# Optimization experiments

Measured on AMD Instinct MI355X. Metric: run time of the kernel, lower is better.

Reference implementation:

```python
import jax, jax.numpy as jnp
import numpy as np

SIGMA = 1e-2        # softness of the silhouette edge test, in NDC units (~1 pixel)
VIEW_ANGLE_DEG = 30.0  # NMR default perspective viewing angle
DIST_THRESHOLD = 6.0
EPS = 1e-7


def _normalize(v):
    return v / jnp.maximum(jnp.linalg.norm(v), 1e-8)


def setup_inputs() -> dict:
    key = jax.random.key(0)
    k1, k2, k3 = jax.random.split(key, 3)
    V, F, H, W = 1024, 2048, 192, 192
    vertices = 2.0 * jax.random.normal(k1, (1, V, 3), dtype=jnp.float32)
    faces = jax.random.randint(k2, (1, F, 3), 0, V, dtype=jnp.int32)
    image_ref = (jax.random.uniform(k3, (H, W), dtype=jnp.float32) > 0.5).astype(jnp.float32)
    camera_position = jnp.array([6.0, 10.0, -14.0], dtype=jnp.float32)
    return {"vertices": vertices, "faces": faces, "image_ref": image_ref,
            "camera_position": camera_position}


def _render_silhouette(vertices, faces, camera_position, H, W):
    dt = vertices.dtype
    # ---- look_at camera transform (NMR convention: at=origin, up=+y) ----
    eye = camera_position
    z_axis = _normalize(-eye)                      # toward the origin
    x_axis = _normalize(jnp.cross(jnp.array([0., 1., 0.], dt), z_axis))
    y_axis = jnp.cross(z_axis, x_axis)
    R = jnp.stack([x_axis, y_axis, z_axis])        # [3,3], rows = camera axes
    v_cam = (vertices[0] - eye) @ R.T              # [V,3]
    # ---- perspective projection to NDC ----
    ratio = jnp.tan(jnp.deg2rad(jnp.asarray(VIEW_ANGLE_DEG, dt)))
    z = jnp.maximum(v_cam[:, 2], 1e-5)
    xy = v_cam[:, :2] / (z[:, None] * ratio)       # [V,2] in [-1,1]
    # ---- gather per-face screen-space vertices ----
    fv = xy[faces[0]]                              # [F,3,2]  irregular gather
    edges = fv[:, [1, 2, 0], :] - fv               # [F,3,2]  edge vectors
    # edge-function constant: cross(edge, p - v) = ex*py - ey*px + (ey*vx - ex*vy)
    c = edges[..., 1] * fv[..., 0] - edges[..., 0] * fv[..., 1]          # [F,3]
    elen = jnp.maximum(jnp.linalg.norm(edges, axis=-1), 1e-8)            # [F,3]
    # orientation sign from signed twice-area so either winding counts as inside
    e01, e02 = fv[:, 1] - fv[:, 0], fv[:, 2] - fv[:, 0]
    area2 = e01[:, 0] * e02[:, 1] - e01[:, 1] * e02[:, 0]                # [F]
    sgn = jnp.where(area2 >= 0, 1.0, -1.0).astype(dt)                    # [F]
    # ---- pixel grid (NDC centers) ----
    xs = (jnp.arange(W, dtype=dt) + 0.5) / W * 2.0 - 1.0
    ys = 1.0 - (jnp.arange(H, dtype=dt) + 0.5) / H * 2.0
    px = xs[None, :]                               # broadcast to [H,W]
    py = ys[:, None]
    # ---- soft inside test: product of per-edge sigmoids of signed distance ----
    inside = jnp.ones((faces.shape[1], H, W), dt)
    for i in range(3):  # fixed small structural loop over triangle edges
        d = (edges[:, i, 0, None, None] * py
             - edges[:, i, 1, None, None] * px
             + c[:, i, None, None])                # [F,H,W]
        d = d * (sgn / elen[:, i])[:, None, None]  # normalized signed distance
        inside = inside * jax.nn.sigmoid(d / SIGMA)
    # silhouette = 1 - prod_f (1 - inside_f), accumulated in log space
    log_miss = jnp.sum(jnp.log(1.0 - inside + EPS), axis=0)  # [H,W]
    return 1.0 - jnp.exp(log_miss)


def reference(vertices, faces, image_ref, camera_position):
    H, W = image_ref.shape
    image = _render_silhouette(vertices, faces, camera_position, H, W)   # [H,W]
    distance = jnp.linalg.norm(camera_position)
    distance_penalty = jax.nn.relu(DIST_THRESHOLD - distance)
    loss = jnp.sum((image_ref - image) ** 2) * (1.0 + distance_penalty)
    return loss
```

## Files before the change

### kernel.cpp

```cpp
#include <hip/hip_runtime.h>

#define HH 192
#define WW 192
#define VV 1024
#define FF 2048
#define NPIX (HH*WW)
#define SIG 0.01f
#define EPSF 1e-7f
#define LOG2E 1.4426950408889634f
#define BAND_T 15.0f
#define C_OUT 1.4426943e-7f
#define C_IN  (-23.2534966642f)
#define NTILE 576


__global__ void __launch_bounds__(256)
prep_kernel(const float* __restrict__ verts, const int* __restrict__ faces,
            const float* __restrict__ cam, float* __restrict__ coeffs,
            float* __restrict__ logmiss, float* __restrict__ factor_out,
            float* __restrict__ out) {
    const int b = blockIdx.x, tid = threadIdx.x;
    if (b < NPIX / 256) {
        logmiss[b * 256 + tid] = 0.0f;
        return;
    }
    __shared__ float sx[VV], sy[VV];
    const float cx = cam[0], cy = cam[1], cz = cam[2];
    const float nrm = sqrtf(cx*cx + cy*cy + cz*cz);
    const float inv = 1.0f / fmaxf(nrm, 1e-8f);
    const float zx = -cx*inv, zy = -cy*inv, zz = -cz*inv;
    float xx = zz, xz = -zx;
    const float invx = 1.0f / fmaxf(sqrtf(xx*xx + xz*xz), 1e-8f);
    xx *= invx; xz *= invx;
    const float yx = zy*xz;
    const float yy = zz*xx - zx*xz;
    const float yz = -zy*xx;
    const float ratio = 0.57735026918962576f;

    for (int i = tid; i < VV; i += 256) {
        const float vx = verts[3*i+0] - cx;
        const float vy = verts[3*i+1] - cy;
        const float vz = verts[3*i+2] - cz;
        const float pcx = xx*vx + xz*vz;
        const float pcy = yx*vx + yy*vy + yz*vz;
        float pcz = zx*vx + zy*vy + zz*vz;
        pcz = fmaxf(pcz, 1e-5f);
        const float iz = 1.0f / (pcz * ratio);
        sx[i] = pcx * iz;
        sy[i] = pcy * iz;
    }
    __syncthreads();

    const int f = (b - 144) * 256 + tid;
    const int i0 = faces[3*f+0], i1 = faces[3*f+1], i2 = faces[3*f+2];
    const float p0x = sx[i0], p0y = sy[i0];
    const float p1x = sx[i1], p1y = sy[i1];
    const float p2x = sx[i2], p2y = sy[i2];
    const float e0x = p1x-p0x, e0y = p1y-p0y;
    const float e1x = p2x-p1x, e1y = p2y-p1y;
    const float e2x = p0x-p2x, e2y = p0y-p2y;
    const float c0 = e0y*p0x - e0x*p0y;
    const float c1 = e1y*p1x - e1x*p1y;
    const float c2 = e2y*p2x - e2x*p2y;
    const float area2 = e0x*(p2y-p0y) - e0y*(p2x-p0x);
    const float sgn = (area2 >= 0.0f) ? 1.0f : -1.0f;
    const float l0 = fmaxf(sqrtf(e0x*e0x + e0y*e0y), 1e-8f);
    const float l1 = fmaxf(sqrtf(e1x*e1x + e1y*e1y), 1e-8f);
    const float l2 = fmaxf(sqrtf(e2x*e2x + e2y*e2y), 1e-8f);
    const float m0 = -sgn * (LOG2E/SIG) / l0;
    const float m1 = -sgn * (LOG2E/SIG) / l1;
    const float m2 = -sgn * (LOG2E/SIG) / l2;
    coeffs[0*FF+f] = m0*e0x;  coeffs[1*FF+f] = -m0*e0y;  coeffs[2*FF+f] = m0*c0;
    coeffs[3*FF+f] = m1*e1x;  coeffs[4*FF+f] = -m1*e1y;  coeffs[5*FF+f] = m1*c1;
    coeffs[6*FF+f] = m2*e2x;  coeffs[7*FF+f] = -m2*e2y;  coeffs[8*FF+f] = m2*c2;

    if (b == 144 && tid == 0) {
        const float dist = sqrtf(cx*cx + cy*cy + cz*cz);
        *factor_out = 1.0f + fmaxf(6.0f - dist, 0.0f);
        *out = 0.0f;
    }
}

__global__ void __launch_bounds__(256)
main_kernel(const float* __restrict__ coeffs, float* __restrict__ logmiss) {
    const int t = blockIdx.x;
    const int w = threadIdx.x >> 6, l = threadIdx.x & 63;
    const int chunk = blockIdx.y * 4 + w;
    const int f = chunk * 64 + l;

    const int tx = t % 24, ty = t / 24;
    const int x = tx*8 + (l & 7), y = ty*8 + (l >> 3);
    const float px = (x + 0.5f) * (2.0f/WW) - 1.0f;
    const float py = 1.0f - (y + 0.5f) * (2.0f/HH);
    const float xc = (tx*8 + 4.0f) * (2.0f/WW) - 1.0f;
    const float yc = 1.0f - (ty*8 + 4.0f) * (2.0f/HH);
    const float hx = 3.5f * (2.0f/WW), hy = 3.5f * (2.0f/HH);
    const float dIn = C_IN - C_OUT;

    const float A0 = coeffs[0*FF+f], B0 = coeffs[1*FF+f], C0 = coeffs[2*FF+f];
    const float A1 = coeffs[3*FF+f], B1 = coeffs[4*FF+f], C1 = coeffs[5*FF+f];
    const float A2 = coeffs[6*FF+f], B2 = coeffs[7*FF+f], C2 = coeffs[8*FF+f];
    const float ac0 = fmaf(A0, yc, fmaf(B0, xc, C0));
    const float ac1 = fmaf(A1, yc, fmaf(B1, xc, C1));
    const float ac2 = fmaf(A2, yc, fmaf(B2, xc, C2));
    const float sp0 = fmaf(fabsf(A0), hy, fabsf(B0)*hx);
    const float sp1 = fmaf(fabsf(A1), hy, fabsf(B1)*hx);
    const float sp2 = fmaf(fabsf(A2), hy, fabsf(B2)*hx);
    const bool skip = (ac0 - sp0 >= BAND_T) || (ac1 - sp1 >= BAND_T) || (ac2 - sp2 >= BAND_T);
    const bool deep = (ac0 + sp0 <= -BAND_T) && (ac1 + sp1 <= -BAND_T) && (ac2 + sp2 <= -BAND_T);

    float acc = 64.0f * C_OUT + (float)__popcll(__ballot(deep)) * dIn;
    unsigned long long mb = __ballot(!skip && !deep);
    while (mb) {
        const int src = __builtin_ctzll(mb); mb &= mb - 1;
#define RL(v) __int_as_float(__builtin_amdgcn_readlane(__float_as_int(v), src))
        const float a0 = fmaf(RL(A0), py, fmaf(RL(B0), px, RL(C0)));
        const float a1 = fmaf(RL(A1), py, fmaf(RL(B1), px, RL(C1)));
        const float a2 = fmaf(RL(A2), py, fmaf(RL(B2), px, RL(C2)));
#undef RL
        const float t0 = __builtin_amdgcn_exp2f(a0);
        const float t1 = __builtin_amdgcn_exp2f(a1);
        const float t2 = __builtin_amdgcn_exp2f(a2);
        const float P = (1.0f + t0) * (1.0f + t1) * (1.0f + t2);
        const float v = (1.0f + EPSF) - __builtin_amdgcn_rcpf(P);
        acc += __builtin_amdgcn_logf(v) - C_OUT;
    }
    atomicAdd(&logmiss[t*64 + l], acc);
}

__global__ void __launch_bounds__(256)
loss_kernel(const float* __restrict__ logmiss, const float* __restrict__ ref,
            const float* __restrict__ factor, float* __restrict__ out) {
    const int p = blockIdx.x * 256 + threadIdx.x;
    const int w = p >> 6, l = p & 63;
    const int x = (w % 24) * 8 + (l & 7);
    const int y = (w / 24) * 8 + (l >> 3);
    const float s = logmiss[p];
    const float image = 1.0f - __builtin_amdgcn_exp2f(s);
    const float d = ref[y*WW + x] - image;
    float sq = d * d;
    #pragma unroll
    for (int off = 32; off > 0; off >>= 1)
        sq += __shfl_down(sq, off, 64);
    __shared__ float wsum[4];
    const int lane = threadIdx.x & 63, wave = threadIdx.x >> 6;
    if (lane == 0) wsum[wave] = sq;
    __syncthreads();
    if (threadIdx.x == 0) {
        const float tot = (wsum[0] + wsum[1] + wsum[2] + wsum[3]) * factor[0];
        atomicAdd(out, tot);
    }
}

extern "C" void kernel_launch(void* const* d_in, const int* in_sizes, int n_in,
                              void* d_out, int out_size, void* d_ws, size_t ws_size,
                              hipStream_t stream) {
    const float* verts = (const float*)d_in[0];
    const int*   faces = (const int*)d_in[1];
    const float* ref   = (const float*)d_in[2];
    const float* cam   = (const float*)d_in[3];
    float* out = (float*)d_out;

    float* ws      = (float*)d_ws;
    float* logmiss = ws;
    float* coeffs  = ws + NPIX;
    float* factor  = ws + NPIX + 9*FF;

    prep_kernel<<<152, 256, 0, stream>>>(verts, faces, cam, coeffs,
                                         logmiss, factor, out);
    main_kernel<<<dim3(NTILE, 8), 256, 0, stream>>>(coeffs, logmiss);
    loss_kernel<<<NPIX/256, 256, 0, stream>>>(logmiss, ref, factor, out);
}
```

Measured before the change: 86.07 us.

## Fuse prep, raster and loss into one kernel with per-tile face recompute

```diff
diff --git a/kernel.cpp b/kernel.cpp
--- a/kernel.cpp
+++ b/kernel.cpp
@@ -4,7 +4,6 @@
 #define WW 192
 #define VV 1024
 #define FF 2048
-#define NPIX (HH*WW)
 #define SIG 0.01f
 #define EPSF 1e-7f
 #define LOG2E 1.4426950408889634f
@@ -13,18 +12,14 @@
 #define C_IN  (-23.2534966642f)
 #define NTILE 576
 
+__global__ void __launch_bounds__(256)
+fused_kernel(const float* __restrict__ verts, const int* __restrict__ faces,
+             const float* __restrict__ ref, const float* __restrict__ cam,
+             float* __restrict__ out) {
+    __shared__ float sx[VV], sy[VV];
+    __shared__ float red[4][64];
+    const int tid = threadIdx.x;
 
-__global__ void __launch_bounds__(256)
-prep_kernel(const float* __restrict__ verts, const int* __restrict__ faces,
-            const float* __restrict__ cam, float* __restrict__ coeffs,
-            float* __restrict__ logmiss, float* __restrict__ factor_out,
-            float* __restrict__ out) {
-    const int b = blockIdx.x, tid = threadIdx.x;
-    if (b < NPIX / 256) {
-        logmiss[b * 256 + tid] = 0.0f;
-        return;
-    }
-    __shared__ float sx[VV], sy[VV];
     const float cx = cam[0], cy = cam[1], cz = cam[2];
     const float nrm = sqrtf(cx*cx + cy*cy + cz*cz);
     const float inv = 1.0f / fmaxf(nrm, 1e-8f);
@@ -32,9 +27,7 @@
     float xx = zz, xz = -zx;
     const float invx = 1.0f / fmaxf(sqrtf(xx*xx + xz*xz), 1e-8f);
     xx *= invx; xz *= invx;
-    const float yx = zy*xz;
-    const float yy = zz*xx - zx*xz;
-    const float yz = -zy*xx;
+    const float yx = zy*xz, yy = zz*xx - zx*xz, yz = -zy*xx;
     const float ratio = 0.57735026918962576f;
 
     for (int i = tid; i < VV; i += 256) {
@@ -51,44 +44,8 @@
     }
     __syncthreads();
 
-    const int f = (b - 144) * 256 + tid;
-    const int i0 = faces[3*f+0], i1 = faces[3*f+1], i2 = faces[3*f+2];
-    const float p0x = sx[i0], p0y = sy[i0];
-    const float p1x = sx[i1], p1y = sy[i1];
-    const float p2x = sx[i2], p2y = sy[i2];
-    const float e0x = p1x-p0x, e0y = p1y-p0y;
-    const float e1x = p2x-p1x, e1y = p2y-p1y;
-    const float e2x = p0x-p2x, e2y = p0y-p2y;
-    const float c0 = e0y*p0x - e0x*p0y;
-    const float c1 = e1y*p1x - e1x*p1y;
-    const float c2 = e2y*p2x - e2x*p2y;
-    const float area2 = e0x*(p2y-p0y) - e0y*(p2x-p0x);
-    const float sgn = (area2 >= 0.0f) ? 1.0f : -1.0f;
-    const float l0 = fmaxf(sqrtf(e0x*e0x + e0y*e0y), 1e-8f);
-    const float l1 = fmaxf(sqrtf(e1x*e1x + e1y*e1y), 1e-8f);
-    const float l2 = fmaxf(sqrtf(e2x*e2x + e2y*e2y), 1e-8f);
-    const float m0 = -sgn * (LOG2E/SIG) / l0;
-    const float m1 = -sgn * (LOG2E/SIG) / l1;
-    const float m2 = -sgn * (LOG2E/SIG) / l2;
-    coeffs[0*FF+f] = m0*e0x;  coeffs[1*FF+f] = -m0*e0y;  coeffs[2*FF+f] = m0*c0;
-    coeffs[3*FF+f] = m1*e1x;  coeffs[4*FF+f] = -m1*e1y;  coeffs[5*FF+f] = m1*c1;
-    coeffs[6*FF+f] = m2*e2x;  coeffs[7*FF+f] = -m2*e2y;  coeffs[8*FF+f] = m2*c2;
-
-    if (b == 144 && tid == 0) {
-        const float dist = sqrtf(cx*cx + cy*cy + cz*cz);
-        *factor_out = 1.0f + fmaxf(6.0f - dist, 0.0f);
-        *out = 0.0f;
-    }
-}
-
-__global__ void __launch_bounds__(256)
-main_kernel(const float* __restrict__ coeffs, float* __restrict__ logmiss) {
-    const int t = blockIdx.x;
-    const int w = threadIdx.x >> 6, l = threadIdx.x & 63;
-    const int chunk = blockIdx.y * 4 + w;
-    const int f = chunk * 64 + l;
-
-    const int tx = t % 24, ty = t / 24;
+    const int t = blockIdx.x, tx = t % 24, ty = t / 24;
+    const int w = tid >> 6, l = tid & 63;
     const int x = tx*8 + (l & 7), y = ty*8 + (l >> 3);
     const float px = (x + 0.5f) * (2.0f/WW) - 1.0f;
     const float py = 1.0f - (y + 0.5f) * (2.0f/HH);
@@ -96,59 +53,76 @@
     const float yc = 1.0f - (ty*8 + 4.0f) * (2.0f/HH);
     const float hx = 3.5f * (2.0f/WW), hy = 3.5f * (2.0f/HH);
     const float dIn = C_IN - C_OUT;
+    const float kk = -(LOG2E / SIG);
 
-    const float A0 = coeffs[0*FF+f], B0 = coeffs[1*FF+f], C0 = coeffs[2*FF+f];
-    const float A1 = coeffs[3*FF+f], B1 = coeffs[4*FF+f], C1 = coeffs[5*FF+f];
-    const float A2 = coeffs[6*FF+f], B2 = coeffs[7*FF+f], C2 = coeffs[8*FF+f];
-    const float ac0 = fmaf(A0, yc, fmaf(B0, xc, C0));
-    const float ac1 = fmaf(A1, yc, fmaf(B1, xc, C1));
-    const float ac2 = fmaf(A2, yc, fmaf(B2, xc, C2));
-    const float sp0 = fmaf(fabsf(A0), hy, fabsf(B0)*hx);
-    const float sp1 = fmaf(fabsf(A1), hy, fabsf(B1)*hx);
-    const float sp2 = fmaf(fabsf(A2), hy, fabsf(B2)*hx);
-    const bool skip = (ac0 - sp0 >= BAND_T) || (ac1 - sp1 >= BAND_T) || (ac2 - sp2 >= BAND_T);
-    const bool deep = (ac0 + sp0 <= -BAND_T) && (ac1 + sp1 <= -BAND_T) && (ac2 + sp2 <= -BAND_T);
+    float acc = 512.0f * C_OUT;
+    for (int r = 0; r < 8; ++r) {
+        const int f = (w*8 + r)*64 + l;
+        const int i0 = faces[3*f+0], i1 = faces[3*f+1], i2 = faces[3*f+2];
+        const float p0x = sx[i0], p0y = sy[i0];
+        const float p1x = sx[i1], p1y = sy[i1];
+        const float p2x = sx[i2], p2y = sy[i2];
+        const float e0x = p1x-p0x, e0y = p1y-p0y;
+        const float e1x = p2x-p1x, e1y = p2y-p1y;
+        const float e2x = p0x-p2x, e2y = p0y-p2y;
+        const float c0 = e0y*p0x - e0x*p0y;
+        const float c1 = e1y*p1x - e1x*p1y;
+        const float c2 = e2y*p2x - e2x*p2y;
+        const float area2 = e0x*(p2y-p0y) - e0y*(p2x-p0x);
+        const float sgn = (area2 >= 0.0f) ? kk : -kk;
+        const float m0 = sgn * __builtin_amdgcn_rsqf(fmaxf(e0x*e0x+e0y*e0y, 1e-16f));
+        const float m1 = sgn * __builtin_amdgcn_rsqf(fmaxf(e1x*e1x+e1y*e1y, 1e-16f));
+        const float m2 = sgn * __builtin_amdgcn_rsqf(fmaxf(e2x*e2x+e2y*e2y, 1e-16f));
+        const float A0 = m0*e0x, B0 = -m0*e0y, C0 = m0*c0;
+        const float A1 = m1*e1x, B1 = -m1*e1y, C1 = m1*c1;
+        const float A2 = m2*e2x, B2 = -m2*e2y, C2 = m2*c2;
+        const float ac0 = fmaf(A0, yc, fmaf(B0, xc, C0));
+        const float ac1 = fmaf(A1, yc, fmaf(B1, xc, C1));
+        const float ac2 = fmaf(A2, yc, fmaf(B2, xc, C2));
+        const float sp0 = fmaf(fabsf(A0), hy, fabsf(B0)*hx);
+        const float sp1 = fmaf(fabsf(A1), hy, fabsf(B1)*hx);
+        const float sp2 = fmaf(fabsf(A2), hy, fabsf(B2)*hx);
+        const bool skip = (ac0 - sp0 >= BAND_T) || (ac1 - sp1 >= BAND_T) || (ac2 - sp2 >= BAND_T);
+        const bool deep = (ac0 + sp0 <= -BAND_T) && (ac1 + sp1 <= -BAND_T) && (ac2 + sp2 <= -BAND_T);
+        acc += (float)__popcll(__ballot(deep)) * dIn;
 
-    float acc = 64.0f * C_OUT + (float)__popcll(__ballot(deep)) * dIn;
-    unsigned long long mb = __ballot(!skip && !deep);
-    while (mb) {
-        const int src = __builtin_ctzll(mb); mb &= mb - 1;
+        unsigned long long mb = __ballot(!skip && !deep);
+        float prod = 1.0f;
+        int cnt = 0;
+        while (mb) {
+            const int src = __builtin_ctzll(mb); mb &= mb - 1;
 #define RL(v) __int_as_float(__builtin_amdgcn_readlane(__float_as_int(v), src))
-        const float a0 = fmaf(RL(A0), py, fmaf(RL(B0), px, RL(C0)));
-        const float a1 = fmaf(RL(A1), py, fmaf(RL(B1), px, RL(C1)));
-        const float a2 = fmaf(RL(A2), py, fmaf(RL(B2), px, RL(C2)));
+            const float a0 = fmaf(RL(A0), py, fmaf(RL(B0), px, RL(C0)));
+            const float a1 = fmaf(RL(A1), py, fmaf(RL(B1), px, RL(C1)));
+            const float a2 = fmaf(RL(A2), py, fmaf(RL(B2), px, RL(C2)));
 #undef RL
-        const float t0 = __builtin_amdgcn_exp2f(a0);
-        const float t1 = __builtin_amdgcn_exp2f(a1);
-        const float t2 = __builtin_amdgcn_exp2f(a2);
-        const float P = (1.0f + t0) * (1.0f + t1) * (1.0f + t2);
-        const float v = (1.0f + EPSF) - __builtin_amdgcn_rcpf(P);
-        acc += __builtin_amdgcn_logf(v) - C_OUT;
+            const float t0 = __builtin_amdgcn_exp2f(a0);
+            const float t1 = __builtin_amdgcn_exp2f(a1);
+            const float t2 = __builtin_amdgcn_exp2f(a2);
+            const float P = (1.0f + t0) * (1.0f + t1) * (1.0f + t2);
+            prod *= (1.0f + EPSF) - __builtin_amdgcn_rcpf(P);
+            if (++cnt == 4) {
+                acc += __builtin_amdgcn_logf(prod);
+                prod = 1.0f; cnt = 0;
+            }
+        }
+        if (cnt) acc += __builtin_amdgcn_logf(prod);
     }
-    atomicAdd(&logmiss[t*64 + l], acc);
-}
 
-__global__ void __launch_bounds__(256)
-loss_kernel(const float* __restrict__ logmiss, const float* __restrict__ ref,
-            const float* __restrict__ factor, float* __restrict__ out) {
-    const int p = blockIdx.x * 256 + threadIdx.x;
-    const int w = p >> 6, l = p & 63;
-    const int x = (w % 24) * 8 + (l & 7);
-    const int y = (w / 24) * 8 + (l >> 3);
-    const float s = logmiss[p];
-    const float image = 1.0f - __builtin_amdgcn_exp2f(s);
-    const float d = ref[y*WW + x] - image;
-    float sq = d * d;
-    #pragma unroll
-    for (int off = 32; off > 0; off >>= 1)
-        sq += __shfl_down(sq, off, 64);
-    __shared__ float wsum[4];
-    const int lane = threadIdx.x & 63, wave = threadIdx.x >> 6;
-    if (lane == 0) wsum[wave] = sq;
+    red[w][l] = acc;
     __syncthreads();
-    if (threadIdx.x == 0) {
-        const float tot = (wsum[0] + wsum[1] + wsum[2] + wsum[3]) * factor[0];
-        atomicAdd(out, tot);
+    if (w == 0) {
+        const float S = red[0][l] + red[1][l] + red[2][l] + red[3][l];
+        const float img = 1.0f - __builtin_amdgcn_exp2f(S);
+        const float d = ref[y*WW + x] - img;
+        float sq = d * d;
+        #pragma unroll
+        for (int off = 32; off > 0; off >>= 1)
+            sq += __shfl_down(sq, off, 64);
+        if (l == 0) {
+            const float factor = 1.0f + fmaxf(6.0f - nrm, 0.0f);
+            atomicAdd(out, sq * factor);
+        }
     }
 }
 
@@ -161,13 +135,6 @@
     const float* cam   = (const float*)d_in[3];
     float* out = (float*)d_out;
 
-    float* ws      = (float*)d_ws;
-    float* logmiss = ws;
-    float* coeffs  = ws + NPIX;
-    float* factor  = ws + NPIX + 9*FF;
-
-    prep_kernel<<<152, 256, 0, stream>>>(verts, faces, cam, coeffs,
-                                         logmiss, factor, out);
-    main_kernel<<<dim3(NTILE, 8), 256, 0, stream>>>(coeffs, logmiss);
-    loss_kernel<<<NPIX/256, 256, 0, stream>>>(logmiss, ref, factor, out);
+    hipMemsetAsync(d_out, 0, sizeof(float), stream);
+    fused_kernel<<<NTILE, 256, 0, stream>>>(verts, faces, ref, cam, out);
 }
```

Result: slower. 116.6 us (+35.5%).

## Use fp16 dot2 edge evaluation, batch logs over four faces, tighten band thresholds

Applied to the files above, without the earlier changes.

```diff
diff --git a/kernel.cpp b/kernel.cpp
--- a/kernel.cpp
+++ b/kernel.cpp
@@ -8,10 +8,19 @@
 #define SIG 0.01f
 #define EPSF 1e-7f
 #define LOG2E 1.4426950408889634f
-#define BAND_T 15.0f
+#define SKIP_T 12.5f
+#define DEEP_T 11.0f
 #define C_OUT 1.4426943e-7f
 #define C_IN  (-23.2534966642f)
 #define NTILE 576
+
+#if defined(__has_builtin)
+#if __has_builtin(__builtin_amdgcn_fdot2)
+#define USE_DOT2 1
+#endif
+#endif
+
+typedef _Float16 h2 __attribute__((ext_vector_type(2)));
 
 
 __global__ void __launch_bounds__(256)
@@ -32,9 +41,7 @@
     float xx = zz, xz = -zx;
     const float invx = 1.0f / fmaxf(sqrtf(xx*xx + xz*xz), 1e-8f);
     xx *= invx; xz *= invx;
-    const float yx = zy*xz;
-    const float yy = zz*xx - zx*xz;
-    const float yz = -zy*xx;
+    const float yx = zy*xz, yy = zz*xx - zx*xz, yz = -zy*xx;
     const float ratio = 0.57735026918962576f;
 
     for (int i = tid; i < VV; i += 256) {
@@ -85,8 +92,8 @@
 main_kernel(const float* __restrict__ coeffs, float* __restrict__ logmiss) {
     const int t = blockIdx.x;
     const int w = threadIdx.x >> 6, l = threadIdx.x & 63;
-    const int chunk = blockIdx.y * 4 + w;
-    const int f = chunk * 64 + l;
+    const int c = blockIdx.y * 4 + w;
+    const int f = c * 64 + l;
 
     const int tx = t % 24, ty = t / 24;
     const int x = tx*8 + (l & 7), y = ty*8 + (l >> 3);
@@ -95,7 +102,6 @@
     const float xc = (tx*8 + 4.0f) * (2.0f/WW) - 1.0f;
     const float yc = 1.0f - (ty*8 + 4.0f) * (2.0f/HH);
     const float hx = 3.5f * (2.0f/WW), hy = 3.5f * (2.0f/HH);
-    const float dIn = C_IN - C_OUT;
 
     const float A0 = coeffs[0*FF+f], B0 = coeffs[1*FF+f], C0 = coeffs[2*FF+f];
     const float A1 = coeffs[3*FF+f], B1 = coeffs[4*FF+f], C1 = coeffs[5*FF+f];
@@ -106,25 +112,55 @@
     const float sp0 = fmaf(fabsf(A0), hy, fabsf(B0)*hx);
     const float sp1 = fmaf(fabsf(A1), hy, fabsf(B1)*hx);
     const float sp2 = fmaf(fabsf(A2), hy, fabsf(B2)*hx);
-    const bool skip = (ac0 - sp0 >= BAND_T) || (ac1 - sp1 >= BAND_T) || (ac2 - sp2 >= BAND_T);
-    const bool deep = (ac0 + sp0 <= -BAND_T) && (ac1 + sp1 <= -BAND_T) && (ac2 + sp2 <= -BAND_T);
-
-    float acc = 64.0f * C_OUT + (float)__popcll(__ballot(deep)) * dIn;
+    const bool skip = (ac0 - sp0 >= SKIP_T) || (ac1 - sp1 >= SKIP_T) || (ac2 - sp2 >= SKIP_T);
+    const bool deep = (ac0 + sp0 <= -DEEP_T) && (ac1 + sp1 <= -DEEP_T) && (ac2 + sp2 <= -DEEP_T);
+
+    float acc = 64.0f * C_OUT
+              + (float)__popcll(__ballot(deep)) * (C_IN - C_OUT);
     unsigned long long mb = __ballot(!skip && !deep);
+
+#ifdef USE_DOT2
+    const h2 ab0 = { (_Float16)A0, (_Float16)B0 };
+    const h2 ab1 = { (_Float16)A1, (_Float16)B1 };
+    const h2 ab2 = { (_Float16)A2, (_Float16)B2 };
+    const int pk0 = __builtin_bit_cast(int, ab0);
+    const int pk1 = __builtin_bit_cast(int, ab1);
+    const int pk2 = __builtin_bit_cast(int, ab2);
+    const h2 dyx = { (_Float16)(py - yc), (_Float16)(px - xc) };
+#endif
+
+    float prod = 1.0f;
+    int cnt = 0;
     while (mb) {
         const int src = __builtin_ctzll(mb); mb &= mb - 1;
+#ifdef USE_DOT2
+        const h2 b0 = __builtin_bit_cast(h2, __builtin_amdgcn_readlane(pk0, src));
+        const h2 b1 = __builtin_bit_cast(h2, __builtin_amdgcn_readlane(pk1, src));
+        const h2 b2 = __builtin_bit_cast(h2, __builtin_amdgcn_readlane(pk2, src));
+#define RL(v) __int_as_float(__builtin_amdgcn_readlane(__float_as_int(v), src))
+        const float a0 = __builtin_amdgcn_fdot2(b0, dyx, RL(ac0), false);
+        const float a1 = __builtin_amdgcn_fdot2(b1, dyx, RL(ac1), false);
+        const float a2 = __builtin_amdgcn_fdot2(b2, dyx, RL(ac2), false);
+#undef RL
+#else
 #define RL(v) __int_as_float(__builtin_amdgcn_readlane(__float_as_int(v), src))
         const float a0 = fmaf(RL(A0), py, fmaf(RL(B0), px, RL(C0)));
         const float a1 = fmaf(RL(A1), py, fmaf(RL(B1), px, RL(C1)));
         const float a2 = fmaf(RL(A2), py, fmaf(RL(B2), px, RL(C2)));
 #undef RL
+#endif
         const float t0 = __builtin_amdgcn_exp2f(a0);
         const float t1 = __builtin_amdgcn_exp2f(a1);
         const float t2 = __builtin_amdgcn_exp2f(a2);
-        const float P = (1.0f + t0) * (1.0f + t1) * (1.0f + t2);
-        const float v = (1.0f + EPSF) - __builtin_amdgcn_rcpf(P);
-        acc += __builtin_amdgcn_logf(v) - C_OUT;
-    }
+        const float Pr = (1.0f + t0) * (1.0f + t1) * (1.0f + t2);
+        prod *= (1.0f + EPSF) - __builtin_amdgcn_rcpf(Pr);
+        if (++cnt == 4) {
+            acc += __builtin_amdgcn_logf(prod) - 4.0f*C_OUT;
+            prod = 1.0f; cnt = 0;
+        }
+    }
+    if (cnt) acc += __builtin_amdgcn_logf(prod) - (float)cnt*C_OUT;
+
     atomicAdd(&logmiss[t*64 + l], acc);
 }
 
```

Result: faster. 83.23 us (-3.3%).
